# Kernel tuning notes

Measured on AMD Instinct MI355X. Metric: run time of the kernel, lower is better.

Reference implementation:

```python
import jax, jax.numpy as jnp
import numpy as np

B, T, D = 1024, 512, 128  # batch, history length, embedding = num_units


def setup_inputs() -> dict:
    key = jax.random.key(0)
    ks = jax.random.split(key, 5)
    s = 1.0 / np.sqrt(2 * D)
    return {
        "rnn_input": jax.random.normal(ks[0], (B, T, D), jnp.float32),
        "att_score": jax.random.uniform(ks[1], (B, T, 1), jnp.float32),
        "gate_kernel": jax.random.normal(ks[2], (2 * D, 2 * D), jnp.float32) * s,
        "gate_bias": jnp.ones((2 * D,), jnp.float32),  # TF GRUCell init: gate bias = 1.0
        "cand_kernel": jax.random.normal(ks[3], (2 * D, D), jnp.float32) * s,
        "cand_bias": jnp.zeros((D,), jnp.float32),
        "sequence_length": jax.random.randint(ks[4], (B, 1), 1, T + 1, jnp.int32),
    }


def reference(rnn_input, att_score, gate_kernel, gate_bias, cand_kernel, cand_bias, sequence_length):
    # AUGRU (VecAttGRUCell) dynamic_rnn, return_sequence=True
    Bv, Tv, Dv = rnn_input.shape
    lens = sequence_length.reshape(Bv)                      # tf.squeeze
    x_t = jnp.transpose(rnn_input, (1, 0, 2))               # [T,B,D]
    a_t = jnp.transpose(att_score, (1, 0, 2))               # [T,B,1]
    mask = (jnp.arange(Tv)[:, None] < lens[None, :])[..., None]  # [T,B,1] bool
    h0 = jnp.zeros((Bv, Dv), rnn_input.dtype)

    def step(h, xs):
        x, a, m = xs
        gi = jnp.concatenate([x, h], -1) @ gate_kernel + gate_bias
        r, u = jnp.split(jax.nn.sigmoid(gi), 2, axis=-1)
        c = jnp.tanh(jnp.concatenate([x, r * h], -1) @ cand_kernel + cand_bias)
        u = (1.0 - a) * u                                   # attention-gated update
        new_h = u * h + (1.0 - u) * c
        h_next = jnp.where(m, new_h, h)                     # state copy-through past length
        out = jnp.where(m, new_h, 0.0)                      # dynamic_rnn zeros past length
        return h_next, out

    _, outs = jax.lax.scan(step, h0, (x_t, a_t, mask))
    return jnp.transpose(outs, (1, 0, 2))                   # [B,T,D]
```

## Files before the change

### kernel.cpp

```cpp
#include <hip/hip_runtime.h>
#include <hip/hip_bf16.h>


#define Bn 1024
#define Tn 512
#define Dn 128

typedef __attribute__((ext_vector_type(8))) short short8;
typedef __attribute__((ext_vector_type(4))) short short4v;
typedef __attribute__((ext_vector_type(4))) float f32x4;

#define HS 132
#define BS 136

#define NL2E  (-1.4426950408889634f)
#define N2L2E (-2.8853900817779268f)

__device__ __forceinline__ short f2bf(float f) {
    __hip_bfloat16 h = __float2bfloat16(f);
    return __builtin_bit_cast(short, h);
}
__device__ __forceinline__ unsigned cvt_pk_bf16(float a, float b) {
    unsigned r;
    asm("v_cvt_pk_bf16_f32 %0, %1, %2" : "=v"(r) : "v"(a), "v"(b));
    return r;
}

__device__ __forceinline__ void barrier_lds() {
    __builtin_amdgcn_sched_barrier(0);
    asm volatile("s_waitcnt lgkmcnt(0)" ::: "memory");
    __builtin_amdgcn_s_barrier();
    __builtin_amdgcn_sched_barrier(0);
}

#define MFMA_(a, b, c) __builtin_amdgcn_mfma_f32_16x16x32_bf16((a), (b), (c), 0, 0, 0)

__launch_bounds__(512, 2)
__global__ void augru_kernel(const float* __restrict__ X,
                             const float* __restrict__ ATT,
                             const float* __restrict__ GK,
                             const float* __restrict__ GB,
                             const float* __restrict__ CK,
                             const float* __restrict__ CB,
                             const int*   __restrict__ SL,
                             float* __restrict__ OUT) {
    __shared__ short hb [16 * BS];
    __shared__ short rhb[16 * BS];
    __shared__ short xb [2][16 * BS];
    __shared__ float hf [16 * HS];
    __shared__ float ub [16 * HS];
    __shared__ float abuf[2][16];
    __shared__ int   lenbuf[16];

    const int tid  = threadIdx.x;
    const int wid  = tid >> 6;
    const int lane = tid & 63;
    const int lm   = lane & 15;
    const int q    = lane >> 4;
    const int b0   = blockIdx.x * 16;

    short8 fgx[2][4], fgh[2][4], fcx[4], fch[4];
    const int gcolb = 32 * wid + lm;
    const int ccol  = 16 * wid + lm;
#pragma unroll
    for (int ns = 0; ns < 2; ++ns) {
        const int col = gcolb + 16 * ns;
#pragma unroll
        for (int ks = 0; ks < 4; ++ks) {
            short8 vx, vh;
#pragma unroll
            for (int j = 0; j < 8; ++j) {
                const int k = ks * 32 + q * 8 + j;
                vx[j] = f2bf(GK[k * 256 + col]);
                vh[j] = f2bf(GK[(128 + k) * 256 + col]);
            }
            fgx[ns][ks] = vx; fgh[ns][ks] = vh;
        }
    }
#pragma unroll
    for (int ks = 0; ks < 4; ++ks) {
        short8 vx, vh;
#pragma unroll
        for (int j = 0; j < 8; ++j) {
            const int k = ks * 32 + q * 8 + j;
            vx[j] = f2bf(CK[k * 128 + ccol]);
            vh[j] = f2bf(CK[(128 + k) * 128 + ccol]);
        }
        fcx[ks] = vx; fch[ks] = vh;
    }
    const float pb0 = GB[gcolb]      * NL2E;
    const float pb1 = GB[gcolb + 16] * NL2E;
    const float cbp = CB[ccol]       * N2L2E;

    for (int i = tid; i < 16 * HS; i += 512) hf[i] = 0.0f;
    for (int i = tid; i < 16 * BS; i += 512) hb[i] = 0;
    if (tid < 16) {
        lenbuf[tid]  = SL[b0 + tid];
        abuf[0][tid] = ATT[(size_t)(b0 + tid) * Tn];
    }
    const int prow = tid >> 5;
    const int pcol = (tid & 31) * 4;
    {
        float4 v = *(const float4*)(X + ((size_t)(b0 + prow) * Tn + 0) * Dn + pcol);
        short4v s; s[0] = f2bf(v.x); s[1] = f2bf(v.y); s[2] = f2bf(v.z); s[3] = f2bf(v.w);
        *(short4v*)&xb[0][prow * BS + pcol] = s;
    }
    __syncthreads();

    int len_i[4];
#pragma unroll
    for (int i = 0; i < 4; ++i) len_i[i] = lenbuf[q * 4 + i];

    f32x4 gxA0 = {0.f,0.f,0.f,0.f}, gxA1 = {0.f,0.f,0.f,0.f}, cxA = {0.f,0.f,0.f,0.f};
    f32x4 gxB0, gxB1, cxB;
    {
        short8 ax0[4];
#pragma unroll
        for (int ks = 0; ks < 4; ++ks)
            ax0[ks] = *(const short8*)&xb[0][lm * BS + ks * 32 + q * 8];
#pragma unroll
        for (int ks = 0; ks < 4; ++ks) {
            gxA0 = MFMA_(ax0[ks], fgx[0][ks], gxA0);
            gxA1 = MFMA_(ax0[ks], fgx[1][ks], gxA1);
            cxA  = MFMA_(ax0[ks], fcx[ks],  cxA);
        }
        float4 v = *(const float4*)(X + ((size_t)(b0 + prow) * Tn + 1) * Dn + pcol);
        short4v s; s[0] = f2bf(v.x); s[1] = f2bf(v.y); s[2] = f2bf(v.z); s[3] = f2bf(v.w);
        *(short4v*)&xb[1][prow * BS + pcol] = s;
    }
    __syncthreads();

#define STEP_BODY(t, GIN0, GIN1, CIN, GOUT0, GOUT1, COUT)                         \
    {                                                                             \
        const int cur = (t) & 1, nxt = cur ^ 1;                                   \
        const int tp1 = ((t) + 1 < Tn) ? (t) + 1 : Tn - 1;                        \
        const int tp2 = ((t) + 2 < Tn) ? (t) + 2 : Tn - 1;                        \
        float4 xpre = *(const float4*)(X + ((size_t)(b0 + prow) * Tn + tp2) * Dn + pcol); \
        float  apre = (tid < 16) ? ATT[(size_t)(b0 + tid) * Tn + tp1] : 0.0f;     \
                                  \
        short8 axn[4], ah[4];                                                     \
        _Pragma("unroll")                                                         \
        for (int ks = 0; ks < 4; ++ks) {                                          \
            axn[ks] = *(const short8*)&xb[nxt][lm * BS + ks * 32 + q * 8];        \
            ah[ks]  = *(const short8*)&hb[lm * BS + ks * 32 + q * 8];             \
        }                                                                         \
         \
        f32x4 g0 = GIN0, g1 = GIN1;                                               \
        f32x4 ngx0 = {0.f,0.f,0.f,0.f}, ngx1 = {0.f,0.f,0.f,0.f};                 \
        f32x4 ncx  = {0.f,0.f,0.f,0.f};                                           \
        _Pragma("unroll")                                                         \
        for (int ks = 0; ks < 4; ++ks) {                                          \
            g0 = MFMA_(ah[ks], fgh[0][ks], g0);                                   \
            g1 = MFMA_(ah[ks], fgh[1][ks], g1);                                   \
        }                                                                         \
        _Pragma("unroll")                                                         \
        for (int ks = 0; ks < 4; ++ks) {                                          \
            ngx0 = MFMA_(axn[ks], fgx[0][ks], ngx0);                              \
            ngx1 = MFMA_(axn[ks], fgx[1][ks], ngx1);                              \
            ncx  = MFMA_(axn[ks], fcx[ks],  ncx);                                 \
        }                                                                         \
                            \
        if (wid < 4) {                     \
            const int col0 = 32 * wid + lm;                                       \
            _Pragma("unroll")                                                     \
            for (int i = 0; i < 4; ++i) {                                         \
                const int row = q * 4 + i;                                        \
                const float e0 = __builtin_amdgcn_exp2f(fmaf(g0[i], NL2E, pb0));  \
                const float e1 = __builtin_amdgcn_exp2f(fmaf(g1[i], NL2E, pb1));  \
                const float rh0 = __builtin_amdgcn_rcpf(1.0f + e0) * hf[row * HS + col0];      \
                const float rh1 = __builtin_amdgcn_rcpf(1.0f + e1) * hf[row * HS + col0 + 16]; \
                const unsigned p = cvt_pk_bf16(rh0, rh1);                         \
                rhb[row * BS + col0]      = (short)p;                             \
                rhb[row * BS + col0 + 16] = (short)(p >> 16);                     \
            }                                                                     \
        } else {                                             \
            const int cu0 = 32 * (wid - 4) + lm;                                  \
            float am[4];                                                          \
            _Pragma("unroll")                                                     \
            for (int i = 0; i < 4; ++i) am[i] = 1.0f - abuf[cur][q * 4 + i];      \
            _Pragma("unroll")                                                     \
            for (int i = 0; i < 4; ++i) {                                         \
                const int row = q * 4 + i;                                        \
                const float e0 = __builtin_amdgcn_exp2f(fmaf(g0[i], NL2E, pb0));  \
                const float e1 = __builtin_amdgcn_exp2f(fmaf(g1[i], NL2E, pb1));  \
                ub[row * HS + cu0]      = am[i] * __builtin_amdgcn_rcpf(1.0f + e0); \
                ub[row * HS + cu0 + 16] = am[i] * __builtin_amdgcn_rcpf(1.0f + e1); \
            }                                                                     \
        }                                                                         \
        barrier_lds();                                                            \
                               \
        f32x4 cc = CIN;                                                           \
        _Pragma("unroll")                                                         \
        for (int ks = 0; ks < 4; ++ks) {                                          \
            short8 arh = *(const short8*)&rhb[lm * BS + ks * 32 + q * 8];         \
            cc = MFMA_(arh, fch[ks], cc);                                         \
        }                                                                         \
                                                           \
        float hxv[4];                                                             \
        _Pragma("unroll")                                                         \
        for (int i = 0; i < 4; ++i) {                                             \
            const int row = q * 4 + i;                                            \
            const float e  = __builtin_amdgcn_exp2f(fmaf(cc[i], N2L2E, cbp));     \
            const float cv = fmaf(2.0f, __builtin_amdgcn_rcpf(1.0f + e), -1.0f);  \
            const float up   = ub[row * HS + ccol];                               \
            const float hold = hf[row * HS + ccol];                               \
            const float hn   = fmaf(up, hold - cv, cv);                           \
            const bool valid = ((t) < len_i[i]);                                  \
            const float hnext = valid ? hn : hold;                                \
            OUT[((size_t)(b0 + row) * Tn + (t)) * Dn + ccol] = valid ? hn : 0.0f; \
            hf[row * HS + ccol] = hnext;                                          \
            hxv[i] = hnext;                                                       \
        }                                                                         \
        {                                                                         \
            const unsigned pA = cvt_pk_bf16(hxv[0], hxv[1]);                      \
            const unsigned pB = cvt_pk_bf16(hxv[2], hxv[3]);                      \
            hb[(q * 4 + 0) * BS + ccol] = (short)pA;                              \
            hb[(q * 4 + 1) * BS + ccol] = (short)(pA >> 16);                      \
            hb[(q * 4 + 2) * BS + ccol] = (short)pB;                              \
            hb[(q * 4 + 3) * BS + ccol] = (short)(pB >> 16);                      \
        }                                                                         \
                            \
        {                                                                         \
            uint2 pp;                                                             \
            pp.x = cvt_pk_bf16(xpre.x, xpre.y);                                   \
            pp.y = cvt_pk_bf16(xpre.z, xpre.w);                                   \
            *(uint2*)&xb[cur][prow * BS + pcol] = pp;                             \
            if (tid < 16) abuf[nxt][tid] = apre;                                  \
        }                                                                         \
        barrier_lds();                                                            \
        GOUT0 = ngx0; GOUT1 = ngx1; COUT = ncx;                                   \
    }

    for (int t = 0; t < Tn; t += 2) {
        STEP_BODY(t,     gxA0, gxA1, cxA, gxB0, gxB1, cxB)
        STEP_BODY(t + 1, gxB0, gxB1, cxB, gxA0, gxA1, cxA)
    }
#undef STEP_BODY
}

extern "C" void kernel_launch(void* const* d_in, const int* in_sizes, int n_in,
                              void* d_out, int out_size, void* d_ws, size_t ws_size,
                              hipStream_t stream) {
    (void)in_sizes; (void)n_in; (void)d_ws; (void)ws_size; (void)out_size;
    const float* X   = (const float*)d_in[0];
    const float* ATT = (const float*)d_in[1];
    const float* GK  = (const float*)d_in[2];
    const float* GB  = (const float*)d_in[3];
    const float* CK  = (const float*)d_in[4];
    const float* CB  = (const float*)d_in[5];
    const int*   SL  = (const int*)d_in[6];
    float* OUT = (float*)d_out;

    augru_kernel<<<dim3(Bn / 16), dim3(512), 0, stream>>>(X, ATT, GK, GB, CK, CB, SL, OUT);
}
```

Before: 587.6 us.

## Keep hidden state in registers by aligning gate columns with each wave's output columns

Gate weight columns are remapped so each wave computes the r and u gates for exactly the 16 hidden columns it later updates. This lets the fp32 hidden state and the update gate stay in registers, removing the hf/ub LDS arrays and their reads and writes. The r/u split across wave halves goes away, and every wave now does both sigmoid pairs. Launch bounds drop to one block per SM to make room for the extra weight fragments, which may reduce occupancy.

```diff
diff --git a/kernel.cpp b/kernel.cpp
--- a/kernel.cpp
+++ b/kernel.cpp
@@ -7,10 +7,8 @@
 #define Dn 128
 
 typedef __attribute__((ext_vector_type(8))) short short8;
-typedef __attribute__((ext_vector_type(4))) short short4v;
 typedef __attribute__((ext_vector_type(4))) float f32x4;
 
-#define HS 132
 #define BS 136
 
 #define NL2E  (-1.4426950408889634f)
@@ -25,7 +23,6 @@
     asm("v_cvt_pk_bf16_f32 %0, %1, %2" : "=v"(r) : "v"(a), "v"(b));
     return r;
 }
-
 __device__ __forceinline__ void barrier_lds() {
     __builtin_amdgcn_sched_barrier(0);
     asm volatile("s_waitcnt lgkmcnt(0)" ::: "memory");
@@ -35,7 +32,7 @@
 
 #define MFMA_(a, b, c) __builtin_amdgcn_mfma_f32_16x16x32_bf16((a), (b), (c), 0, 0, 0)
 
-__launch_bounds__(512, 2)
+__launch_bounds__(512, 1)
 __global__ void augru_kernel(const float* __restrict__ X,
                              const float* __restrict__ ATT,
                              const float* __restrict__ GK,
@@ -47,8 +44,6 @@
     __shared__ short hb [16 * BS];
     __shared__ short rhb[16 * BS];
     __shared__ short xb [2][16 * BS];
-    __shared__ float hf [16 * HS];
-    __shared__ float ub [16 * HS];
     __shared__ float abuf[2][16];
     __shared__ int   lenbuf[16];
 
@@ -58,41 +53,29 @@
     const int lm   = lane & 15;
     const int q    = lane >> 4;
     const int b0   = blockIdx.x * 16;
-
-    short8 fgx[2][4], fgh[2][4], fcx[4], fch[4];
-    const int gcolb = 32 * wid + lm;
-    const int ccol  = 16 * wid + lm;
-#pragma unroll
-    for (int ns = 0; ns < 2; ++ns) {
-        const int col = gcolb + 16 * ns;
-#pragma unroll
-        for (int ks = 0; ks < 4; ++ks) {
-            short8 vx, vh;
-#pragma unroll
-            for (int j = 0; j < 8; ++j) {
-                const int k = ks * 32 + q * 8 + j;
-                vx[j] = f2bf(GK[k * 256 + col]);
-                vh[j] = f2bf(GK[(128 + k) * 256 + col]);
-            }
-            fgx[ns][ks] = vx; fgh[ns][ks] = vh;
-        }
-    }
+    const int ccol = 16 * wid + lm;
+
+    short8 fgx0[4], fgx1[4], fgh0[4], fgh1[4], fcx[4], fch[4];
 #pragma unroll
     for (int ks = 0; ks < 4; ++ks) {
-        short8 vx, vh;
+        short8 v0, v1, v2, v3, v4, v5;
 #pragma unroll
         for (int j = 0; j < 8; ++j) {
             const int k = ks * 32 + q * 8 + j;
-            vx[j] = f2bf(CK[k * 128 + ccol]);
-            vh[j] = f2bf(CK[(128 + k) * 128 + ccol]);
+            v0[j] = f2bf(GK[k * 256 + ccol]);
+            v1[j] = f2bf(GK[k * 256 + 128 + ccol]);
+            v2[j] = f2bf(GK[(128 + k) * 256 + ccol]);
+            v3[j] = f2bf(GK[(128 + k) * 256 + 128 + ccol]);
+            v4[j] = f2bf(CK[k * 128 + ccol]);
+            v5[j] = f2bf(CK[(128 + k) * 128 + ccol]);
         }
-        fcx[ks] = vx; fch[ks] = vh;
-    }
-    const float pb0 = GB[gcolb]      * NL2E;
-    const float pb1 = GB[gcolb + 16] * NL2E;
+        fgx0[ks] = v0; fgx1[ks] = v1; fgh0[ks] = v2; fgh1[ks] = v3;
+        fcx[ks] = v4;  fch[ks] = v5;
+    }
+    const float pb0 = GB[ccol]       * NL2E;
+    const float pb1 = GB[128 + ccol] * NL2E;
     const float cbp = CB[ccol]       * N2L2E;
 
-    for (int i = tid; i < 16 * HS; i += 512) hf[i] = 0.0f;
     for (int i = tid; i < 16 * BS; i += 512) hb[i] = 0;
     if (tid < 16) {
         lenbuf[tid]  = SL[b0 + tid];
@@ -102,16 +85,17 @@
     const int pcol = (tid & 31) * 4;
     {
         float4 v = *(const float4*)(X + ((size_t)(b0 + prow) * Tn + 0) * Dn + pcol);
-        short4v s; s[0] = f2bf(v.x); s[1] = f2bf(v.y); s[2] = f2bf(v.z); s[3] = f2bf(v.w);
-        *(short4v*)&xb[0][prow * BS + pcol] = s;
+        uint2 pp; pp.x = cvt_pk_bf16(v.x, v.y); pp.y = cvt_pk_bf16(v.z, v.w);
+        *(uint2*)&xb[0][prow * BS + pcol] = pp;
     }
     __syncthreads();
 
     int len_i[4];
+    float h_reg[4] = {0.f, 0.f, 0.f, 0.f};
 #pragma unroll
     for (int i = 0; i < 4; ++i) len_i[i] = lenbuf[q * 4 + i];
 
-    f32x4 gxA0 = {0.f,0.f,0.f,0.f}, gxA1 = {0.f,0.f,0.f,0.f}, cxA = {0.f,0.f,0.f,0.f};
+    f32x4 gxA0 = {0,0,0,0}, gxA1 = {0,0,0,0}, cxA = {0,0,0,0};
     f32x4 gxB0, gxB1, cxB;
     {
         short8 ax0[4];
@@ -120,13 +104,13 @@
             ax0[ks] = *(const short8*)&xb[0][lm * BS + ks * 32 + q * 8];
 #pragma unroll
         for (int ks = 0; ks < 4; ++ks) {
-            gxA0 = MFMA_(ax0[ks], fgx[0][ks], gxA0);
-            gxA1 = MFMA_(ax0[ks], fgx[1][ks], gxA1);
+            gxA0 = MFMA_(ax0[ks], fgx0[ks], gxA0);
+            gxA1 = MFMA_(ax0[ks], fgx1[ks], gxA1);
             cxA  = MFMA_(ax0[ks], fcx[ks],  cxA);
         }
         float4 v = *(const float4*)(X + ((size_t)(b0 + prow) * Tn + 1) * Dn + pcol);
-        short4v s; s[0] = f2bf(v.x); s[1] = f2bf(v.y); s[2] = f2bf(v.z); s[3] = f2bf(v.w);
-        *(short4v*)&xb[1][prow * BS + pcol] = s;
+        uint2 pp; pp.x = cvt_pk_bf16(v.x, v.y); pp.y = cvt_pk_bf16(v.z, v.w);
+        *(uint2*)&xb[1][prow * BS + pcol] = pp;
     }
     __syncthreads();
 
@@ -146,46 +130,36 @@
         }                                                                         \
          \
         f32x4 g0 = GIN0, g1 = GIN1;                                               \
-        f32x4 ngx0 = {0.f,0.f,0.f,0.f}, ngx1 = {0.f,0.f,0.f,0.f};                 \
-        f32x4 ncx  = {0.f,0.f,0.f,0.f};                                           \
-        _Pragma("unroll")                                                         \
-        for (int ks = 0; ks < 4; ++ks) {                                          \
-            g0 = MFMA_(ah[ks], fgh[0][ks], g0);                                   \
-            g1 = MFMA_(ah[ks], fgh[1][ks], g1);                                   \
-        }                                                                         \
-        _Pragma("unroll")                                                         \
-        for (int ks = 0; ks < 4; ++ks) {                                          \
-            ngx0 = MFMA_(axn[ks], fgx[0][ks], ngx0);                              \
-            ngx1 = MFMA_(axn[ks], fgx[1][ks], ngx1);                              \
-            ncx  = MFMA_(axn[ks], fcx[ks],  ncx);                                 \
-        }                                                                         \
-                            \
-        if (wid < 4) {                     \
-            const int col0 = 32 * wid + lm;                                       \
-            _Pragma("unroll")                                                     \
-            for (int i = 0; i < 4; ++i) {                                         \
-                const int row = q * 4 + i;                                        \
-                const float e0 = __builtin_amdgcn_exp2f(fmaf(g0[i], NL2E, pb0));  \
-                const float e1 = __builtin_amdgcn_exp2f(fmaf(g1[i], NL2E, pb1));  \
-                const float rh0 = __builtin_amdgcn_rcpf(1.0f + e0) * hf[row * HS + col0];      \
-                const float rh1 = __builtin_amdgcn_rcpf(1.0f + e1) * hf[row * HS + col0 + 16]; \
-                const unsigned p = cvt_pk_bf16(rh0, rh1);                         \
-                rhb[row * BS + col0]      = (short)p;                             \
-                rhb[row * BS + col0 + 16] = (short)(p >> 16);                     \
-            }                                                                     \
-        } else {                                             \
-            const int cu0 = 32 * (wid - 4) + lm;                                  \
-            float am[4];                                                          \
-            _Pragma("unroll")                                                     \
-            for (int i = 0; i < 4; ++i) am[i] = 1.0f - abuf[cur][q * 4 + i];      \
-            _Pragma("unroll")                                                     \
-            for (int i = 0; i < 4; ++i) {                                         \
-                const int row = q * 4 + i;                                        \
-                const float e0 = __builtin_amdgcn_exp2f(fmaf(g0[i], NL2E, pb0));  \
-                const float e1 = __builtin_amdgcn_exp2f(fmaf(g1[i], NL2E, pb1));  \
-                ub[row * HS + cu0]      = am[i] * __builtin_amdgcn_rcpf(1.0f + e0); \
-                ub[row * HS + cu0 + 16] = am[i] * __builtin_amdgcn_rcpf(1.0f + e1); \
-            }                                                                     \
+        f32x4 n0 = {0,0,0,0}, n1 = {0,0,0,0}, n2 = {0,0,0,0};                     \
+        _Pragma("unroll")                                                         \
+        for (int ks = 0; ks < 4; ++ks) {                                          \
+            g0 = MFMA_(ah[ks], fgh0[ks], g0);                                     \
+            g1 = MFMA_(ah[ks], fgh1[ks], g1);                                     \
+        }                                                                         \
+        _Pragma("unroll")                                                         \
+        for (int ks = 0; ks < 4; ++ks) {                                          \
+            n0 = MFMA_(axn[ks], fgx0[ks], n0);                                    \
+            n1 = MFMA_(axn[ks], fgx1[ks], n1);                                    \
+            n2 = MFMA_(axn[ks], fcx[ks],  n2);                                    \
+        }                                                                         \
+              \
+        float am[4], up[4], rhv[4];                                               \
+        _Pragma("unroll")                                                         \
+        for (int i = 0; i < 4; ++i) am[i] = 1.0f - abuf[cur][q * 4 + i];          \
+        _Pragma("unroll")                                                         \
+        for (int i = 0; i < 4; ++i) {                                             \
+            const float e0 = __builtin_amdgcn_exp2f(fmaf(g0[i], NL2E, pb0));      \
+            rhv[i] = __builtin_amdgcn_rcpf(1.0f + e0) * h_reg[i];                 \
+            const float e1 = __builtin_amdgcn_exp2f(fmaf(g1[i], NL2E, pb1));      \
+            up[i] = am[i] * __builtin_amdgcn_rcpf(1.0f + e1);                     \
+        }                                                                         \
+        {                                                                         \
+            const unsigned pA_ = cvt_pk_bf16(rhv[0], rhv[1]);                     \
+            const unsigned pB_ = cvt_pk_bf16(rhv[2], rhv[3]);                     \
+            rhb[(q * 4 + 0) * BS + ccol] = (short)pA_;                            \
+            rhb[(q * 4 + 1) * BS + ccol] = (short)(pA_ >> 16);                    \
+            rhb[(q * 4 + 2) * BS + ccol] = (short)pB_;                            \
+            rhb[(q * 4 + 3) * BS + ccol] = (short)(pB_ >> 16);                    \
         }                                                                         \
         barrier_lds();                                                            \
                                \
@@ -195,40 +169,38 @@
             short8 arh = *(const short8*)&rhb[lm * BS + ks * 32 + q * 8];         \
             cc = MFMA_(arh, fch[ks], cc);                                         \
         }                                                                         \
-                                                           \
+                             \
         float hxv[4];                                                             \
         _Pragma("unroll")                                                         \
         for (int i = 0; i < 4; ++i) {                                             \
             const int row = q * 4 + i;                                            \
             const float e  = __builtin_amdgcn_exp2f(fmaf(cc[i], N2L2E, cbp));     \
             const float cv = fmaf(2.0f, __builtin_amdgcn_rcpf(1.0f + e), -1.0f);  \
-            const float up   = ub[row * HS + ccol];                               \
-            const float hold = hf[row * HS + ccol];                               \
-            const float hn   = fmaf(up, hold - cv, cv);                           \
+            const float hn = fmaf(up[i], h_reg[i] - cv, cv);                      \
             const bool valid = ((t) < len_i[i]);                                  \
-            const float hnext = valid ? hn : hold;                                \
+            const float hnext = valid ? hn : h_reg[i];                            \
             OUT[((size_t)(b0 + row) * Tn + (t)) * Dn + ccol] = valid ? hn : 0.0f; \
-            hf[row * HS + ccol] = hnext;                                          \
+            h_reg[i] = hnext;                                                     \
             hxv[i] = hnext;                                                       \
         }                                                                         \
         {                                                                         \
-            const unsigned pA = cvt_pk_bf16(hxv[0], hxv[1]);                      \
-            const unsigned pB = cvt_pk_bf16(hxv[2], hxv[3]);                      \
-            hb[(q * 4 + 0) * BS + ccol] = (short)pA;                              \
-            hb[(q * 4 + 1) * BS + ccol] = (short)(pA >> 16);                      \
-            hb[(q * 4 + 2) * BS + ccol] = (short)pB;                              \
-            hb[(q * 4 + 3) * BS + ccol] = (short)(pB >> 16);                      \
+            const unsigned pA_ = cvt_pk_bf16(hxv[0], hxv[1]);                     \
+            const unsigned pB_ = cvt_pk_bf16(hxv[2], hxv[3]);                     \
+            hb[(q * 4 + 0) * BS + ccol] = (short)pA_;                             \
+            hb[(q * 4 + 1) * BS + ccol] = (short)(pA_ >> 16);                     \
+            hb[(q * 4 + 2) * BS + ccol] = (short)pB_;                             \
+            hb[(q * 4 + 3) * BS + ccol] = (short)(pB_ >> 16);                     \
         }                                                                         \
                             \
         {                                                                         \
-            uint2 pp;                                                             \
-            pp.x = cvt_pk_bf16(xpre.x, xpre.y);                                   \
-            pp.y = cvt_pk_bf16(xpre.z, xpre.w);                                   \
-            *(uint2*)&xb[cur][prow * BS + pcol] = pp;                             \
+            uint2 pp_;                                                            \
+            pp_.x = cvt_pk_bf16(xpre.x, xpre.y);                                  \
+            pp_.y = cvt_pk_bf16(xpre.z, xpre.w);                                  \
+            *(uint2*)&xb[cur][prow * BS + pcol] = pp_;                            \
             if (tid < 16) abuf[nxt][tid] = apre;                                  \
         }                                                                         \
         barrier_lds();                                                            \
-        GOUT0 = ngx0; GOUT1 = ngx1; COUT = ncx;                                   \
+        GOUT0 = n0; GOUT1 = n1; COUT = n2;                                        \
     }
 
     for (int t = 0; t < Tn; t += 2) {
```

After: 526.6 us, median of 2. -10.4%, faster.
